# Kernel optimization log

Hardware: AMD Instinct MI355X
Metric: run time of the kernel (lower is better)

The kernel has to match this reference:

```python
import jax, jax.numpy as jnp
import numpy as np

N, E, C, L, G, O = 100000, 1600000, 128, 7, 2, 40
BETA = 0.9
HEADS, HC = 1, 128  # heads=1, head_channels=hidden_channels=128


def setup_inputs() -> dict:
    key = jax.random.key(0)
    ks = jax.random.split(key, 16)
    s = 0.05  # ~ torch Linear init std for fan_in=128
    inp = {
        'x': jax.random.normal(ks[0], (N, C), jnp.float32),
        'edge_index': jax.random.randint(ks[1], (2, E), 0, N, jnp.int64),
        'Wh': jax.random.normal(ks[2], (L, C, C)) * s,
        'bh': jax.random.normal(ks[3], (L, C)) * s,
        'Wg': jax.random.normal(ks[4], (L, C, C)) * s,
        'bg': jax.random.normal(ks[5], (L, C)) * s,
        'Wl': jax.random.normal(ks[6], (L, C, C)) * s,
        'bl': jax.random.normal(ks[7], (L, C)) * s,
        'ln_g': jnp.ones((L, C)), 'ln_b': jnp.zeros((L, C)),
        'bn_g': jnp.ones((L, C)), 'bn_b': jnp.zeros((L, C)),
        'bn_rm': jnp.zeros((L, C)), 'bn_rv': jnp.ones((L, C)),
        'gWh': jax.random.normal(ks[8], (G, C, C)) * s,
        'gbh': jax.random.normal(ks[9], (G, C)) * s,
        'gWk': jax.random.normal(ks[10], (G, C, C)) * s,
        'gWv': jax.random.normal(ks[11], (G, C, C)) * s,
        'gln_g': jnp.ones((G, C)), 'gln_b': jnp.zeros((G, C)),
        'gWo': jax.random.normal(ks[12], (G, C, C)) * s,
        'gbo': jax.random.normal(ks[13], (G, C)) * s,
        'f_ln_g': jnp.ones((C,)), 'f_ln_b': jnp.zeros((C,)),
        'Wp': jax.random.normal(ks[14], (O, C)) * s,
        'bp': jax.random.normal(ks[15], (O,)) * s,
    }
    return inp


def _layer_norm(x, g, b, eps=1e-5):
    mu = jnp.mean(x, axis=-1, keepdims=True)
    var = jnp.mean((x - mu) ** 2, axis=-1, keepdims=True)
    return (x - mu) * jax.lax.rsqrt(var + eps) * g + b


def reference(x, edge_index, Wh, bh, Wg, bg, Wl, bl, ln_g, ln_b,
              bn_g, bn_b, bn_rm, bn_rv, gWh, gbh, gWk, gWv,
              gln_g, gln_b, gWo, gbo, f_ln_g, f_ln_b, Wp, bp):
    n = x.shape[0]
    src, dst = edge_index[0], edge_index[1]
    # gcn_norm with add_self_loops=True: deg over destination incl. self loop
    deg = jnp.zeros((n,), x.dtype).at[dst].add(1.0) + 1.0
    dinv = jax.lax.rsqrt(deg)
    enorm = (dinv[src] * dinv[dst])[:, None]   # [E,1]
    selfw = (dinv * dinv)[:, None]             # [N,1] self-loop weight

    x_local = jnp.zeros_like(x @ Wh[0].T)
    for i in range(L):
        h = jax.nn.relu(x @ Wh[i].T + bh[i])
        xw = x @ Wg[i].T                                  # GCN lin (bias separate)
        agg = jax.ops.segment_sum(xw[src] * enorm, dst, num_segments=n)
        conv = agg + xw * selfw + bg[i]
        x = conv + x @ Wl[i].T + bl[i]
        # BatchNorm1d in eval mode (running stats)
        x = (x - bn_rm[i]) * jax.lax.rsqrt(bn_rv[i] + 1e-5) * bn_g[i] + bn_b[i]
        x = jax.nn.relu(x)
        x = (1.0 - BETA) * _layer_norm(h * x, ln_g[i], ln_b[i]) + BETA * x
        x_local = x_local + x

    # global linear attention (PolynormerAttention, qk_shared=True, qkv_bias=False)
    xg = _layer_norm(x_local, f_ln_g, f_ln_b)
    for j in range(G):
        h = xg @ gWh[j].T + gbh[j]
        k = jax.nn.sigmoid(xg @ gWk[j].T).reshape(n, HEADS, HC)
        q = k
        v = (xg @ gWv[j].T).reshape(n, HEADS, HC)
        kv = jnp.einsum('ndh,ndm->dhm', k, v)            # [heads,hc,hc]
        num = jnp.einsum('ndh,dhm->ndm', q, kv)          # [N,heads,hc]
        k_sum = jnp.sum(k, axis=0)                       # [heads,hc]
        den = jnp.einsum('ndh,dh->nd', q, k_sum)[..., None]
        attn = (num / (den + 1e-6)).reshape(n, HEADS * HC)
        xg = _layer_norm(attn, gln_g[j], gln_b[j]) * (h + BETA)
        xg = jax.nn.relu(xg @ gWo[j].T + gbo[j])

    return xg @ Wp.T + bp
```

## Files before the change

### kernel.cpp

```cpp
#include <hip/hip_runtime.h>

typedef unsigned short u16;
typedef unsigned int u32;
typedef __attribute__((ext_vector_type(8))) short short8;
typedef __attribute__((ext_vector_type(8))) unsigned short ushort8v;
typedef __attribute__((ext_vector_type(4))) float f32x4;

#define CDIM 128

__device__ __forceinline__ float b2f(u16 u){ return __uint_as_float(((unsigned)u)<<16); }
__device__ __forceinline__ u16 f2b(float f){
  unsigned x = __float_as_uint(f);
  unsigned r = (x + 0x7fffu + ((x>>16)&1u)) >> 16;
  return (u16)r;
}
__device__ __forceinline__ float wsum64(float v){
  #pragma unroll
  for(int d=1; d<64; d<<=1) v += __shfl_xor(v, d, 64);
  return v;
}
__device__ __forceinline__ float wsum16(float v){
  v += __shfl_xor(v, 1, 64);
  v += __shfl_xor(v, 2, 64);
  v += __shfl_xor(v, 4, 64);
  v += __shfl_xor(v, 8, 64);
  return v;
}

__global__ void k_probe(const u32* __restrict__ x, const u32* __restrict__ ei, int* __restrict__ flags){
  __shared__ int s_bf, s_nz;
  if(threadIdx.x == 0){ s_bf = 0; s_nz = 0; }
  __syncthreads();
  int c_bf = 0, c_nz = 0;
  for(int i = threadIdx.x; i < 4096; i += 256){
    u32 w = x[i];
    u32 e = (w >> 7) & 0xFFu;
    if(e >= 100u && e <= 140u) c_bf++;
    if(ei[2*i + 1] != 0u) c_nz++;
  }
  atomicAdd(&s_bf, c_bf);
  atomicAdd(&s_nz, c_nz);
  __syncthreads();
  if(threadIdx.x == 0){
    flags[0] = (s_bf < 2048) ? 1 : 0;
    flags[1] = (s_nz < 8) ? 1 : 0;
  }
}

__global__ void k_cvt_x(const void* __restrict__ src, u16* __restrict__ dst, int n,
                        const int* __restrict__ flags){
  int i = (blockIdx.x*256 + threadIdx.x)*8;
  if(i + 7 >= n) return;
  if(flags[0]){
    const float* s = (const float*)src + i;
    float4 a = *(const float4*)s;
    float4 b = *(const float4*)(s + 4);
    ushort8v o;
    o[0]=f2b(a.x); o[1]=f2b(a.y); o[2]=f2b(a.z); o[3]=f2b(a.w);
    o[4]=f2b(b.x); o[5]=f2b(b.y); o[6]=f2b(b.z); o[7]=f2b(b.w);
    *(ushort8v*)(dst + i) = o;
  } else {
    *(ushort8v*)(dst + i) = *(const ushort8v*)((const u16*)src + i);
  }
}

struct CvtArgs {
  const void* src[24];
  u16* dst[24];
  int n[24];
};

__global__ void k_cvt_params(CvtArgs a, const int* __restrict__ flags){
  int seg = blockIdx.y;
  int i = blockIdx.x*256 + threadIdx.x;
  int n = a.n[seg];
  if(i >= n) return;
  if(flags[0]) a.dst[seg][i] = f2b(((const float*)a.src[seg])[i]);
  else         a.dst[seg][i] = ((const u16*)a.src[seg])[i];
}

__global__ void k_cvt_ei_count(const int* __restrict__ src, int* __restrict__ dst, int E,
                               const int* __restrict__ flags, u32* __restrict__ cnt){
  int i = blockIdx.x*256 + threadIdx.x;
  if(i >= 2*E) return;
  int v = flags[1] ? src[2*i] : src[i];
  dst[i] = v;
  if(i >= E) atomicAdd(&cnt[v], 1u);
}

__global__ __launch_bounds__(256) void k_scan1(const u32* __restrict__ cnt, int n, u32* __restrict__ bsum){
  const int lane = threadIdx.x & 63;
  const int wv = threadIdx.x >> 6;
  int i = blockIdx.x*256 + threadIdx.x;
  u32 v = (i < n) ? cnt[i] : 0u;
  #pragma unroll
  for(int d=1; d<64; d<<=1) v += (u32)__shfl_xor((int)v, d, 64);
  __shared__ u32 ws[4];
  if(lane == 0) ws[wv] = v;
  __syncthreads();
  if(threadIdx.x == 0) bsum[blockIdx.x] = ws[0] + ws[1] + ws[2] + ws[3];
}

__global__ __launch_bounds__(1024) void k_scan2(const u32* __restrict__ bsum, int nb, u32* __restrict__ bpre){
  __shared__ u32 s[1024];
  int t = threadIdx.x;
  u32 v = (t < nb) ? bsum[t] : 0u;
  s[t] = v;
  __syncthreads();
  for(int d=1; d<1024; d<<=1){
    u32 y = (t >= d) ? s[t-d] : 0u;
    __syncthreads();
    s[t] += y;
    __syncthreads();
  }
  if(t < nb) bpre[t] = s[t] - v;
}

__global__ __launch_bounds__(256) void k_scan3(const u32* __restrict__ cnt, int n,
                                               const u32* __restrict__ bpre,
                                               u32* __restrict__ rowstart, u32* __restrict__ cursor,
                                               float* __restrict__ dinv){
  const int lane = threadIdx.x & 63;
  const int wv = threadIdx.x >> 6;
  int i = blockIdx.x*256 + threadIdx.x;
  u32 v = (i < n) ? cnt[i] : 0u;
  u32 x = v;
  #pragma unroll
  for(int d=1; d<64; d<<=1){
    u32 y = (u32)__shfl_up((int)x, d, 64);
    if(lane >= d) x += y;
  }
  __shared__ u32 ws[4];
  if(lane == 63) ws[wv] = x;
  __syncthreads();
  u32 woff = 0;
  #pragma unroll
  for(int w=0; w<4; w++) if(w < wv) woff += ws[w];
  u32 incl = x + woff;
  u32 rs = bpre[blockIdx.x] + incl - v;
  if(i < n){
    rowstart[i] = rs;
    cursor[i] = rs;
    dinv[i] = rsqrtf((float)(v + 1u));
    if(i == n-1) rowstart[n] = rs + v;
  }
}

__global__ __launch_bounds__(256) void k_scatter8(
  const int* __restrict__ ei, int E, int Nn, int nsl,
  u32* __restrict__ cursor, const float* __restrict__ dinv, int2* __restrict__ colw)
{
  const int r = blockIdx.x & 7;
  const int slice = blockIdx.x >> 3;
  const int q = (Nn + 7) >> 3;
  const int lo = r*q;
  const int hi = (lo + q < Nn) ? lo + q : Nn;
  const int chunk = (E + nsl - 1) / nsl;
  int e0 = slice*chunk;
  int e1 = e0 + chunk; if(e1 > E) e1 = E;
  for(int e = e0 + threadIdx.x; e < e1; e += 256){
    int d = ei[E + e];
    if(d >= lo && d < hi){
      int s = ei[e];
      u32 p = atomicAdd(&cursor[d], 1u);
      colw[p] = make_int2(s, __float_as_int(dinv[s]));
    }
  }
}

__global__ __launch_bounds__(256) void k_gemm3(
  const u16* __restrict__ A, int M,
  const u16* __restrict__ W0, const u16* __restrict__ bs0, int op0, u16* __restrict__ O0,
  const u16* __restrict__ W1, const u16* __restrict__ bs1, int op1, u16* __restrict__ O1,
  const u16* __restrict__ W2, const u16* __restrict__ bs2, int op2, u16* __restrict__ O2)
{
  const int lane = threadIdx.x & 63;
  const int wv = threadIdx.x >> 6;
  const int l16 = lane & 15, quad = lane >> 4;
  const long rbase = (long)blockIdx.x*128 + wv*32;

  short8 af[2][4];
  #pragma unroll
  for(int rt=0; rt<2; rt++){
    long r = rbase + rt*16 + l16; if(r >= M) r = M-1;
    const u16* ap = A + r*CDIM + quad*8;
    #pragma unroll
    for(int kt=0; kt<4; kt++)
      af[rt][kt] = *(const short8*)(ap + kt*32);
  }

  const u16* Ws[3] = {W0, W1, W2};
  const u16* Bs[3] = {bs0, bs1, bs2};
  u16* Os[3] = {O0, O1, O2};
  const int ops[3] = {op0, op1, op2};

  for(int w=0; w<3; w++){
    const u16* Wm = Ws[w];
    if(!Wm) break;
    const int op = ops[w];
    u16* Op = Os[w];
    const u16* bp = Bs[w];
    for(int ct=0; ct<8; ct++){
      f32x4 acc0 = {0.f,0.f,0.f,0.f}, acc1 = {0.f,0.f,0.f,0.f};
      const u16* wp = Wm + (ct*16 + l16)*CDIM + quad*8;
      #pragma unroll
      for(int kt=0; kt<4; kt++){
        short8 bf = *(const short8*)(wp + kt*32);
        acc0 = __builtin_amdgcn_mfma_f32_16x16x32_bf16(af[0][kt], bf, acc0, 0, 0, 0);
        acc1 = __builtin_amdgcn_mfma_f32_16x16x32_bf16(af[1][kt], bf, acc1, 0, 0, 0);
      }
      const int col = ct*16 + l16;
      const float bias = bp ? b2f(bp[col]) : 0.f;
      #pragma unroll
      for(int rt=0; rt<2; rt++){
        f32x4 a = rt ? acc1 : acc0;
        #pragma unroll
        for(int g=0; g<4; g++){
          long r = rbase + rt*16 + quad*4 + g;
          if(r < M){
            float v = a[g] + bias;
            if(op == 1) v = fmaxf(v, 0.f);
            else if(op == 2) v = 1.f/(1.f + __expf(-v));
            Op[r*CDIM + col] = f2b(v);
          }
        }
      }
    }
  }
}

__global__ __launch_bounds__(256) void k_layer_epi(
  const u16* __restrict__ xw, const u16* __restrict__ h, const u16* __restrict__ xl,
  const int2* __restrict__ colw, const u32* __restrict__ rowstart, const float* __restrict__ dinv,
  const u16* __restrict__ bg, const u16* __restrict__ bng, const u16* __restrict__ bnb,
  const u16* __restrict__ bnrm, const u16* __restrict__ bnrv,
  const u16* __restrict__ lng, const u16* __restrict__ lnb,
  float* __restrict__ xlocal, u16* __restrict__ xout, int n, int first)
{
  const int lane = threadIdx.x & 63;
  const int node = blockIdx.x*4 + (threadIdx.x >> 6);
  if(node >= n) return;
  const int c0 = lane*2;
  u32 j0 = rowstart[node], j1 = rowstart[node+1];
  float a0 = 0.f, a1 = 0.f;
  for(u32 base = j0; base < j1; base += 64){
    int avail = (int)(j1 - base);
    int cnt = avail < 64 ? avail : 64;
    int2 pw = make_int2(0, 0);
    if(lane < cnt) pw = colw[base + lane];
    int cntp = (cnt + 15) & ~15;
    for(int t = 0; t < cntp; t += 16){
      int s[16]; float w[16]; ushort2 v[16];
      #pragma unroll
      for(int k2=0;k2<16;k2++){
        s[k2] = __shfl(pw.x, t+k2, 64);
        w[k2] = __int_as_float(__shfl(pw.y, t+k2, 64));
      }
      #pragma unroll
      for(int k2=0;k2<16;k2++) v[k2] = *(const ushort2*)(xw + (size_t)s[k2]*CDIM + c0);
      #pragma unroll
      for(int k2=0;k2<16;k2++){
        a0 = fmaf(w[k2], b2f(v[k2].x), a0);
        a1 = fmaf(w[k2], b2f(v[k2].y), a1);
      }
    }
  }
  float dn = dinv[node], sw = dn*dn;
  size_t base = (size_t)node*CDIM + c0;
  ushort2 xwv = *(const ushort2*)(xw + base);
  ushort2 xlv = *(const ushort2*)(xl + base);
  ushort2 hv  = *(const ushort2*)(h  + base);
  float x10 = a0*dn + b2f(xwv.x)*sw + b2f(bg[c0])   + b2f(xlv.x);
  float x11 = a1*dn + b2f(xwv.y)*sw + b2f(bg[c0+1]) + b2f(xlv.y);
  float s0 = rsqrtf(b2f(bnrv[c0])   + 1e-5f) * b2f(bng[c0]);
  float s1 = rsqrtf(b2f(bnrv[c0+1]) + 1e-5f) * b2f(bng[c0+1]);
  float x20 = (x10 - b2f(bnrm[c0]))*s0   + b2f(bnb[c0]);
  float x21 = (x11 - b2f(bnrm[c0+1]))*s1 + b2f(bnb[c0+1]);
  float x30 = fmaxf(x20, 0.f);
  float x31 = fmaxf(x21, 0.f);
  float t0 = b2f(hv.x)*x30, t1 = b2f(hv.y)*x31;
  float mu = wsum64(t0 + t1) * (1.f/128.f);
  float d0 = t0 - mu, d1 = t1 - mu;
  float var = wsum64(d0*d0 + d1*d1) * (1.f/128.f);
  float inv = rsqrtf(var + 1e-5f);
  float y0 = d0*inv*b2f(lng[c0])   + b2f(lnb[c0]);
  float y1 = d1*inv*b2f(lng[c0+1]) + b2f(lnb[c0+1]);
  float xn0 = 0.1f*y0 + 0.9f*x30;
  float xn1 = 0.1f*y1 + 0.9f*x31;
  float2 xl2;
  if(first){
    xl2.x = xn0; xl2.y = xn1;
  } else {
    xl2 = *(float2*)(xlocal + base);
    xl2.x += xn0; xl2.y += xn1;
  }
  *(float2*)(xlocal + base) = xl2;
  ushort2 o; o.x = f2b(xn0); o.y = f2b(xn1);
  *(ushort2*)(xout + base) = o;
}

__global__ __launch_bounds__(256) void k_ln(
  const float* __restrict__ xin, const u16* __restrict__ g, const u16* __restrict__ b,
  u16* __restrict__ out, int n)
{
  const int lane = threadIdx.x & 63;
  const int node = blockIdx.x*4 + (threadIdx.x >> 6);
  if(node >= n) return;
  const int c0 = lane*2;
  size_t base = (size_t)node*CDIM + c0;
  float2 v = *(const float2*)(xin + base);
  float mu = wsum64(v.x + v.y) * (1.f/128.f);
  float d0 = v.x - mu, d1 = v.y - mu;
  float var = wsum64(d0*d0 + d1*d1) * (1.f/128.f);
  float inv = rsqrtf(var + 1e-5f);
  ushort2 o;
  o.x = f2b(d0*inv*b2f(g[c0])   + b2f(b[c0]));
  o.y = f2b(d1*inv*b2f(g[c0+1]) + b2f(b[c0+1]));
  *(ushort2*)(out + base) = o;
}

__global__ __launch_bounds__(256) void k_kv(
  const u16* __restrict__ kk, const u16* __restrict__ vv, int n, int npb,
  float* __restrict__ part)
{
  __shared__ float sk[8][128];
  __shared__ float sv[8][128];
  const int tid = threadIdx.x;
  const int tr = tid >> 4, tc = tid & 15;
  float acc[8][8];
  #pragma unroll
  for(int i=0;i<8;i++){
    #pragma unroll
    for(int j=0;j<8;j++) acc[i][j] = 0.f;
  }
  float ks[8];
  #pragma unroll
  for(int i=0;i<8;i++) ks[i] = 0.f;
  int start = blockIdx.x * npb;
  int end = start + npb; if(end > n) end = n;
  const int lr = tid >> 5;
  const int lc = (tid & 31) * 4;
  for(int g0 = start; g0 < end; g0 += 8){
    int cnt = end - g0; if(cnt > 8) cnt = 8;
    __syncthreads();
    if(lr < cnt){
      ushort4 kq = *(const ushort4*)(kk + (size_t)(g0+lr)*CDIM + lc);
      ushort4 vq = *(const ushort4*)(vv + (size_t)(g0+lr)*CDIM + lc);
      sk[lr][lc] = b2f(kq.x); sk[lr][lc+1] = b2f(kq.y); sk[lr][lc+2] = b2f(kq.z); sk[lr][lc+3] = b2f(kq.w);
      sv[lr][lc] = b2f(vq.x); sv[lr][lc+1] = b2f(vq.y); sv[lr][lc+2] = b2f(vq.z); sv[lr][lc+3] = b2f(vq.w);
    }
    __syncthreads();
    for(int r=0; r<cnt; r++){
      float4 ka = *(const float4*)&sk[r][tr*8];
      float4 kb = *(const float4*)&sk[r][tr*8+4];
      float4 va = *(const float4*)&sv[r][tc*8];
      float4 vb = *(const float4*)&sv[r][tc*8+4];
      float kr[8] = {ka.x,ka.y,ka.z,ka.w,kb.x,kb.y,kb.z,kb.w};
      float vr[8] = {va.x,va.y,va.z,va.w,vb.x,vb.y,vb.z,vb.w};
      #pragma unroll
      for(int i=0;i<8;i++){
        #pragma unroll
        for(int j=0;j<8;j++) acc[i][j] = fmaf(kr[i], vr[j], acc[i][j]);
      }
      if(tc == 0){
        #pragma unroll
        for(int i=0;i<8;i++) ks[i] += kr[i];
      }
    }
  }
  float* p = part + (size_t)blockIdx.x * 16512;
  #pragma unroll
  for(int i=0;i<8;i++){
    #pragma unroll
    for(int j=0;j<8;j++)
      p[(size_t)(tc*8+j)*CDIM + tr*8 + i] = acc[i][j];
  }
  if(tc == 0){
    #pragma unroll
    for(int i=0;i<8;i++) p[16384 + tr*8 + i] = ks[i];
  }
}

__global__ void k_kvred(const float* __restrict__ part, int nb, u16* __restrict__ Bext){
  int i = blockIdx.x*256 + threadIdx.x;
  if(i >= 144*128) return;
  float s = 0.f;
  if(i < 16512){
    #pragma unroll 8
    for(int b=0;b<nb;b++) s += part[(size_t)b*16512 + i];
  }
  Bext[i] = f2b(s);
}

__global__ __launch_bounds__(256) void k_attn(
  const u16* __restrict__ q, const u16* __restrict__ Bext, const u16* __restrict__ hg,
  const u16* __restrict__ g, const u16* __restrict__ b,
  u16* __restrict__ out, int M)
{
  const int lane = threadIdx.x & 63;
  const int wv = threadIdx.x >> 6;
  const int l16 = lane & 15, quad = lane >> 4;
  const long rbase = (long)blockIdx.x*128 + wv*32;

  short8 af[2][4];
  #pragma unroll
  for(int rt=0; rt<2; rt++){
    long r = rbase + rt*16 + l16; if(r >= M) r = M-1;
    const u16* ap = q + r*CDIM + quad*8;
    #pragma unroll
    for(int kt=0; kt<4; kt++)
      af[rt][kt] = *(const short8*)(ap + kt*32);
  }
  f32x4 acc[2][9];
  f32x4 zero = {0.f,0.f,0.f,0.f};
  #pragma unroll
  for(int rt=0; rt<2; rt++){
    #pragma unroll
    for(int ct=0; ct<9; ct++) acc[rt][ct] = zero;
  }
  #pragma unroll
  for(int ct=0; ct<9; ct++){
    const u16* wp = Bext + (ct*16 + l16)*CDIM + quad*8;
    #pragma unroll
    for(int kt=0; kt<4; kt++){
      short8 bf = *(const short8*)(wp + kt*32);
      acc[0][ct] = __builtin_amdgcn_mfma_f32_16x16x32_bf16(af[0][kt], bf, acc[0][ct], 0, 0, 0);
      acc[1][ct] = __builtin_amdgcn_mfma_f32_16x16x32_bf16(af[1][kt], bf, acc[1][ct], 0, 0, 0);
    }
  }
  #pragma unroll
  for(int rt=0; rt<2; rt++){
    float rden[4];
    #pragma unroll
    for(int gi=0; gi<4; gi++){
      float dv = __shfl(acc[rt][8][gi], lane & 48, 64);
      rden[gi] = 1.f/(dv + 1e-6f);
    }
    #pragma unroll
    for(int gi=0; gi<4; gi++){
      float sum = 0.f;
      #pragma unroll
      for(int ct=0; ct<8; ct++) sum += acc[rt][ct][gi]*rden[gi];
      float mu = wsum16(sum) * (1.f/128.f);
      float vs = 0.f;
      #pragma unroll
      for(int ct=0; ct<8; ct++){ float d = acc[rt][ct][gi]*rden[gi] - mu; vs = fmaf(d, d, vs); }
      float inv = rsqrtf(wsum16(vs)*(1.f/128.f) + 1e-5f);
      long r = rbase + rt*16 + quad*4 + gi;
      if(r < M){
        #pragma unroll
        for(int ct=0; ct<8; ct++){
          int col = ct*16 + l16;
          float y = (acc[rt][ct][gi]*rden[gi] - mu)*inv*b2f(g[col]) + b2f(b[col]);
          float hvv = b2f(hg[(size_t)r*CDIM + col]);
          out[(size_t)r*CDIM + col] = f2b(y*(hvv + 0.9f));
        }
      }
    }
  }
}

__global__ __launch_bounds__(256) void k_gout(
  const u16* __restrict__ A, const u16* __restrict__ W, const u16* __restrict__ bs,
  void* __restrict__ outv, int M, const int* __restrict__ flags)
{
  const int lane = threadIdx.x & 63;
  const int wv = threadIdx.x >> 6;
  const int l16 = lane & 15, quad = lane >> 4;
  const long rbase = (long)blockIdx.x*128 + wv*32;
  const int f32m = flags[0];
  short8 af[2][4];
  #pragma unroll
  for(int rt=0; rt<2; rt++){
    long r = rbase + rt*16 + l16; if(r >= M) r = M-1;
    const u16* ap = A + r*CDIM + quad*8;
    #pragma unroll
    for(int kt=0; kt<4; kt++)
      af[rt][kt] = *(const short8*)(ap + kt*32);
  }
  f32x4 acc[2][3];
  f32x4 zero = {0.f,0.f,0.f,0.f};
  #pragma unroll
  for(int rt=0; rt<2; rt++){
    #pragma unroll
    for(int ct=0; ct<3; ct++) acc[rt][ct] = zero;
  }
  #pragma unroll
  for(int ct=0; ct<3; ct++){
    int row = ct*16 + l16; if(row > 39) row = 39;
    const u16* wp = W + row*CDIM + quad*8;
    #pragma unroll
    for(int kt=0; kt<4; kt++){
      short8 bf = *(const short8*)(wp + kt*32);
      acc[0][ct] = __builtin_amdgcn_mfma_f32_16x16x32_bf16(af[0][kt], bf, acc[0][ct], 0, 0, 0);
      acc[1][ct] = __builtin_amdgcn_mfma_f32_16x16x32_bf16(af[1][kt], bf, acc[1][ct], 0, 0, 0);
    }
  }
  #pragma unroll
  for(int ct=0; ct<3; ct++){
    int col = ct*16 + l16;
    if(col < 40){
      float bias = b2f(bs[col]);
      #pragma unroll
      for(int rt=0; rt<2; rt++){
        #pragma unroll
        for(int gi=0; gi<4; gi++){
          long r = rbase + rt*16 + quad*4 + gi;
          if(r < M){
            float v = acc[rt][ct][gi] + bias;
            if(f32m) ((float*)outv)[r*40 + col] = v;
            else     ((u16*)outv)[r*40 + col] = f2b(v);
          }
        }
      }
    }
  }
}

extern "C" void kernel_launch(void* const* d_in, const int* in_sizes, int n_in,
                              void* d_out, int out_size, void* d_ws, size_t ws_size,
                              hipStream_t stream)
{
  (void)n_in;
  const int C = CDIM;
  const int Nn = in_sizes[0] / C;
  const int E  = in_sizes[1] / 2;

  char* ws = (char*)d_ws;
  size_t off = 0;
  auto alloc = [&](size_t bytes) -> char* {
    char* p = ws + off;
    off = (off + bytes + 255) & ~(size_t)255;
    return p;
  };
  u16*   x_cur  = (u16*)  alloc((size_t)Nn*C*2);
  float* xlocal = (float*)alloc((size_t)Nn*C*4);
  u16*   hb     = (u16*)  alloc((size_t)Nn*C*2);
  u16*   xwb    = (u16*)  alloc((size_t)Nn*C*2);
  u16*   xlb    = (u16*)  alloc((size_t)Nn*C*2);
  float* dinv   = (float*)alloc((size_t)Nn*4);
  u32*   cnt    = (u32*)  alloc((size_t)Nn*4);
  u32*   rowst  = (u32*)  alloc((size_t)(Nn+1)*4);
  u32*   cursor = (u32*)  alloc((size_t)Nn*4);
  int2*  colw   = (int2*) alloc((size_t)E*8);
  u16*   Bext   = (u16*)  alloc((size_t)144*128*2);
  int*   flags  = (int*)  alloc(256);
  u32*   bsum   = (u32*)  alloc(1024*4);
  u32*   bpre   = (u32*)  alloc(1024*4);
  size_t ptot = 0;
  for(int k=2;k<26;k++) ptot += (size_t)in_sizes[k];
  u16* pbuf = (u16*)alloc(ptot*2);

  if(off > ws_size){
    hipMemsetAsync(d_out, 0, (size_t)out_size*2, stream);
    return;
  }

  const u16* pp[26];
  {
    size_t po = 0;
    for(int k=2;k<26;k++){ pp[k] = pbuf + po; po += (size_t)in_sizes[k]; }
  }
  const u16* cWh  = pp[2];  const u16* cbh  = pp[3];
  const u16* cWg  = pp[4];  const u16* cbg  = pp[5];
  const u16* cWl  = pp[6];  const u16* cbl  = pp[7];
  const u16* clng = pp[8];  const u16* clnb = pp[9];
  const u16* cbng = pp[10]; const u16* cbnb = pp[11];
  const u16* cbnrm= pp[12]; const u16* cbnrv= pp[13];
  const u16* cgWh = pp[14]; const u16* cgbh = pp[15];
  const u16* cgWk = pp[16]; const u16* cgWv = pp[17];
  const u16* cglng= pp[18]; const u16* cglnb= pp[19];
  const u16* cgWo = pp[20]; const u16* cgbo = pp[21];
  const u16* cflng= pp[22]; const u16* cflnb= pp[23];
  const u16* cWp  = pp[24]; const u16* cbp  = pp[25];

  u16* xb  = (u16*)xlocal;
  int* eib = (int*)((char*)xlocal + (size_t)Nn*C*2);
  u16* xg  = x_cur;
  float* kvpart = xlocal;

  const int NB_KV = 512;
  const int npb = (Nn + NB_KV - 1) / NB_KV;
  const int gblk = (Nn + 127) / 128;
  const int nodeblk = (Nn + 3) / 4;
  const int nscan = (Nn + 255) / 256;
  const int NSL = 512;

  k_probe<<<1, 256, 0, stream>>>((const u32*)d_in[0], (const u32*)d_in[1], flags);
  hipMemsetAsync(cnt, 0, (size_t)Nn*4, stream);
  k_cvt_ei_count<<<(2*E + 255)/256, 256, 0, stream>>>((const int*)d_in[1], eib, E, flags, cnt);
  k_cvt_x<<<(Nn*C/8 + 255)/256, 256, 0, stream>>>(d_in[0], xb, Nn*C, flags);
  {
    CvtArgs a;
    int maxn = 0;
    for(int k=2;k<26;k++){
      a.src[k-2] = d_in[k];
      a.dst[k-2] = (u16*)pp[k];
      a.n[k-2]   = in_sizes[k];
      if(in_sizes[k] > maxn) maxn = in_sizes[k];
    }
    dim3 g((maxn + 255)/256, 24);
    k_cvt_params<<<g, 256, 0, stream>>>(a, flags);
  }

  k_scan1<<<nscan, 256, 0, stream>>>(cnt, Nn, bsum);
  k_scan2<<<1, 1024, 0, stream>>>(bsum, nscan, bpre);
  k_scan3<<<nscan, 256, 0, stream>>>(cnt, Nn, bpre, rowst, cursor, dinv);
  k_scatter8<<<NSL*8, 256, 0, stream>>>(eib, E, Nn, NSL, cursor, dinv, colw);

  const u16* xa = xb;
  for(int i=0; i<7; i++){
    k_gemm3<<<gblk, 256, 0, stream>>>(xa, Nn,
        cWh + (size_t)i*C*C, cbh + (size_t)i*C, 1, hb,
        cWg + (size_t)i*C*C, (const u16*)nullptr, 0, xwb,
        cWl + (size_t)i*C*C, cbl + (size_t)i*C, 0, xlb);
    k_layer_epi<<<nodeblk, 256, 0, stream>>>(xwb, hb, xlb, colw, rowst, dinv,
        cbg + (size_t)i*C, cbng + (size_t)i*C, cbnb + (size_t)i*C,
        cbnrm + (size_t)i*C, cbnrv + (size_t)i*C,
        clng + (size_t)i*C, clnb + (size_t)i*C,
        xlocal, x_cur, Nn, (i==0) ? 1 : 0);
    xa = x_cur;
  }

  k_ln<<<nodeblk, 256, 0, stream>>>(xlocal, cflng, cflnb, xg, Nn);

  for(int j=0; j<2; j++){
    k_gemm3<<<gblk, 256, 0, stream>>>(xg, Nn,
        cgWh + (size_t)j*C*C, cgbh + (size_t)j*C, 0, hb,
        cgWk + (size_t)j*C*C, (const u16*)nullptr, 2, xwb,
        cgWv + (size_t)j*C*C, (const u16*)nullptr, 0, xlb);
    k_kv   <<<NB_KV, 256, 0, stream>>>(xwb, xlb, Nn, npb, kvpart);
    k_kvred<<<(144*128 + 255)/256, 256, 0, stream>>>(kvpart, NB_KV, Bext);
    k_attn <<<gblk, 256, 0, stream>>>(xwb, Bext, hb, cglng + (size_t)j*C, cglnb + (size_t)j*C, xlb, Nn);
    k_gemm3<<<gblk, 256, 0, stream>>>(xlb, Nn,
        cgWo + (size_t)j*C*C, cgbo + (size_t)j*C, 1, xg,
        (const u16*)nullptr, (const u16*)nullptr, 0, (u16*)nullptr,
        (const u16*)nullptr, (const u16*)nullptr, 0, (u16*)nullptr);
  }

  k_gout<<<gblk, 256, 0, stream>>>(xg, cWp, cbp, d_out, Nn, flags);
}
```

Before: 1.767 ms.

## Stage GEMM outputs through LDS and fuse final LayerNorm into last layer

```diff
diff --git a/kernel.cpp b/kernel.cpp
--- a/kernel.cpp
+++ b/kernel.cpp
@@ -174,6 +174,7 @@
   const u16* __restrict__ W1, const u16* __restrict__ bs1, int op1, u16* __restrict__ O1,
   const u16* __restrict__ W2, const u16* __restrict__ bs2, int op2, u16* __restrict__ O2)
 {
+  __shared__ u16 tile[128*136];
   const int lane = threadIdx.x & 63;
   const int wv = threadIdx.x >> 6;
   const int l16 = lane & 15, quad = lane >> 4;
@@ -193,6 +194,9 @@
   const u16* Bs[3] = {bs0, bs1, bs2};
   u16* Os[3] = {O0, O1, O2};
   const int ops[3] = {op0, op1, op2};
+
+  const int rl = threadIdx.x >> 4;
+  const int cseg = threadIdx.x & 15;
 
   for(int w=0; w<3; w++){
     const u16* Wm = Ws[w];
@@ -200,30 +204,48 @@
     const int op = ops[w];
     u16* Op = Os[w];
     const u16* bp = Bs[w];
+
+    f32x4 acc[2][8];
+    #pragma unroll
+    for(int rt=0; rt<2; rt++){
+      #pragma unroll
+      for(int ct=0; ct<8; ct++) acc[rt][ct] = (f32x4){0.f,0.f,0.f,0.f};
+    }
+    #pragma unroll
     for(int ct=0; ct<8; ct++){
-      f32x4 acc0 = {0.f,0.f,0.f,0.f}, acc1 = {0.f,0.f,0.f,0.f};
       const u16* wp = Wm + (ct*16 + l16)*CDIM + quad*8;
       #pragma unroll
       for(int kt=0; kt<4; kt++){
         short8 bf = *(const short8*)(wp + kt*32);
-        acc0 = __builtin_amdgcn_mfma_f32_16x16x32_bf16(af[0][kt], bf, acc0, 0, 0, 0);
-        acc1 = __builtin_amdgcn_mfma_f32_16x16x32_bf16(af[1][kt], bf, acc1, 0, 0, 0);
-      }
-      const int col = ct*16 + l16;
-      const float bias = bp ? b2f(bp[col]) : 0.f;
-      #pragma unroll
-      for(int rt=0; rt<2; rt++){
-        f32x4 a = rt ? acc1 : acc0;
+        acc[0][ct] = __builtin_amdgcn_mfma_f32_16x16x32_bf16(af[0][kt], bf, acc[0][ct], 0, 0, 0);
+        acc[1][ct] = __builtin_amdgcn_mfma_f32_16x16x32_bf16(af[1][kt], bf, acc[1][ct], 0, 0, 0);
+      }
+    }
+    if(w) __syncthreads();
+    #pragma unroll
+    for(int rt=0; rt<2; rt++){
+      const int row0 = wv*32 + rt*16 + quad*4;
+      #pragma unroll
+      for(int ct=0; ct<8; ct++){
+        const int col = ct*16 + l16;
+        const float bias = bp ? b2f(bp[col]) : 0.f;
         #pragma unroll
         for(int g=0; g<4; g++){
-          long r = rbase + rt*16 + quad*4 + g;
-          if(r < M){
-            float v = a[g] + bias;
-            if(op == 1) v = fmaxf(v, 0.f);
-            else if(op == 2) v = 1.f/(1.f + __expf(-v));
-            Op[r*CDIM + col] = f2b(v);
-          }
+          float v = acc[rt][ct][g] + bias;
+          if(op == 1) v = fmaxf(v, 0.f);
+          else if(op == 2) v = 1.f/(1.f + __expf(-v));
+          tile[(row0+g)*136 + col] = f2b(v);
         }
+      }
+    }
+    __syncthreads();
+    #pragma unroll
+    for(int p=0; p<8; p++){
+      int row = p*16 + rl;
+      long gr = (long)blockIdx.x*128 + row;
+      if(gr < M){
+        ushort8v vv = *(const ushort8v*)(tile + row*136 + cseg*8);
+        *(ushort8v*)(Op + gr*CDIM + cseg*8) = vv;
       }
     }
   }
@@ -235,7 +257,8 @@
   const u16* __restrict__ bg, const u16* __restrict__ bng, const u16* __restrict__ bnb,
   const u16* __restrict__ bnrm, const u16* __restrict__ bnrv,
   const u16* __restrict__ lng, const u16* __restrict__ lnb,
-  float* __restrict__ xlocal, u16* __restrict__ xout, int n, int first)
+  const u16* __restrict__ flng, const u16* __restrict__ flnb,
+  float* __restrict__ xlocal, u16* __restrict__ xout, int n, int first, int final)
 {
   const int lane = threadIdx.x & 63;
   const int node = blockIdx.x*4 + (threadIdx.x >> 6);
@@ -248,18 +271,18 @@
     int cnt = avail < 64 ? avail : 64;
     int2 pw = make_int2(0, 0);
     if(lane < cnt) pw = colw[base + lane];
-    int cntp = (cnt + 15) & ~15;
-    for(int t = 0; t < cntp; t += 16){
-      int s[16]; float w[16]; ushort2 v[16];
-      #pragma unroll
-      for(int k2=0;k2<16;k2++){
+    int cntp = (cnt + 7) & ~7;
+    for(int t = 0; t < cntp; t += 8){
+      int s[8]; float w[8]; ushort2 v[8];
+      #pragma unroll
+      for(int k2=0;k2<8;k2++){
         s[k2] = __shfl(pw.x, t+k2, 64);
         w[k2] = __int_as_float(__shfl(pw.y, t+k2, 64));
       }
       #pragma unroll
-      for(int k2=0;k2<16;k2++) v[k2] = *(const ushort2*)(xw + (size_t)s[k2]*CDIM + c0);
-      #pragma unroll
-      for(int k2=0;k2<16;k2++){
+      for(int k2=0;k2<8;k2++) v[k2] = *(const ushort2*)(xw + (size_t)s[k2]*CDIM + c0);
+      #pragma unroll
+      for(int k2=0;k2<8;k2++){
         a0 = fmaf(w[k2], b2f(v[k2].x), a0);
         a1 = fmaf(w[k2], b2f(v[k2].y), a1);
       }
@@ -294,29 +317,20 @@
     xl2 = *(float2*)(xlocal + base);
     xl2.x += xn0; xl2.y += xn1;
   }
-  *(float2*)(xlocal + base) = xl2;
-  ushort2 o; o.x = f2b(xn0); o.y = f2b(xn1);
-  *(ushort2*)(xout + base) = o;
-}
-
-__global__ __launch_bounds__(256) void k_ln(
-  const float* __restrict__ xin, const u16* __restrict__ g, const u16* __restrict__ b,
-  u16* __restrict__ out, int n)
-{
-  const int lane = threadIdx.x & 63;
-  const int node = blockIdx.x*4 + (threadIdx.x >> 6);
-  if(node >= n) return;
-  const int c0 = lane*2;
-  size_t base = (size_t)node*CDIM + c0;
-  float2 v = *(const float2*)(xin + base);
-  float mu = wsum64(v.x + v.y) * (1.f/128.f);
-  float d0 = v.x - mu, d1 = v.y - mu;
-  float var = wsum64(d0*d0 + d1*d1) * (1.f/128.f);
-  float inv = rsqrtf(var + 1e-5f);
-  ushort2 o;
-  o.x = f2b(d0*inv*b2f(g[c0])   + b2f(b[c0]));
-  o.y = f2b(d1*inv*b2f(g[c0+1]) + b2f(b[c0+1]));
-  *(ushort2*)(out + base) = o;
+  if(!final){
+    *(float2*)(xlocal + base) = xl2;
+    ushort2 o; o.x = f2b(xn0); o.y = f2b(xn1);
+    *(ushort2*)(xout + base) = o;
+  } else {
+    float mu2 = wsum64(xl2.x + xl2.y) * (1.f/128.f);
+    float e0 = xl2.x - mu2, e1 = xl2.y - mu2;
+    float var2 = wsum64(e0*e0 + e1*e1) * (1.f/128.f);
+    float inv2 = rsqrtf(var2 + 1e-5f);
+    ushort2 o;
+    o.x = f2b(e0*inv2*b2f(flng[c0])   + b2f(flnb[c0]));
+    o.y = f2b(e1*inv2*b2f(flng[c0+1]) + b2f(flnb[c0+1]));
+    *(ushort2*)(xout + base) = o;
+  }
 }
 
 __global__ __launch_bounds__(256) void k_kv(
@@ -618,11 +632,10 @@
         cbg + (size_t)i*C, cbng + (size_t)i*C, cbnb + (size_t)i*C,
         cbnrm + (size_t)i*C, cbnrv + (size_t)i*C,
         clng + (size_t)i*C, clnb + (size_t)i*C,
-        xlocal, x_cur, Nn, (i==0) ? 1 : 0);
+        cflng, cflnb,
+        xlocal, x_cur, Nn, (i==0) ? 1 : 0, (i==6) ? 1 : 0);
     xa = x_cur;
   }
-
-  k_ln<<<nodeblk, 256, 0, stream>>>(xlocal, cflng, cflnb, xg, Nn);
 
   for(int j=0; j<2; j++){
     k_gemm3<<<gblk, 256, 0, stream>>>(xg, Nn,
```

Result: slower. 1.951 ms (+10.4%).
